# Performance work log

Hardware: AMD Instinct MI355X
Metric: run time of the kernel (lower is better)

## Reference

```python
import jax, jax.numpy as jnp
import numpy as np

N_NODES = 100000
D_IN, D_OUT = 1024, 512
B, K = 8192, 64


def setup_inputs() -> dict:
    key = jax.random.key(0)
    k1, k2, k3, k4, k5 = jax.random.split(key, 5)
    X = jax.random.normal(k1, (N_NODES, D_IN), dtype=jnp.float32)
    indices = jax.random.randint(k2, (B, K), 0, N_NODES)  # top-K PPR neighbor ids per batch node
    values = jax.random.uniform(k3, (B, K), dtype=jnp.float32)  # PPR weights
    W = jax.random.normal(k4, (D_IN, D_OUT), dtype=jnp.float32) / np.sqrt(D_IN)
    b = jax.random.normal(k5, (D_OUT,), dtype=jnp.float32)
    return {"X": X, "indices": indices, "values": values, "W": W, "b": b}


def reference(X, indices, values, W, b):
    # Sparse PPR branch. Original: encode only unique gathered rows, then
    # re-expand via inverse indices. Since the encoder is row-pointwise,
    # encoder(X[u_fwd])[u_bwd] == encoder(X)[indices]; we encode all nodes once
    # (n_nodes < B*K here) then gather -- identical math, jit-friendly.
    enc = X @ W + b                      # [N, d_out]
    gathered = enc[indices]              # [B, K, d_out]
    return jnp.einsum('bk,bkd->bd', values, gathered)  # weighted sum over K neighbors
```

## Files before the change

### kernel.cpp

```cpp
#include <hip/hip_runtime.h>

typedef unsigned short ushort_t;
typedef __bf16 bf16x8 __attribute__((ext_vector_type(8)));
typedef float f32x4 __attribute__((ext_vector_type(4)));

#define N_NODES 100000
#define D_IN    1024
#define D_OUT   512
#define B_SZ    8192
#define K_NB    64

__device__ __forceinline__ ushort_t f2bf(float f) {
    unsigned int u = __builtin_bit_cast(unsigned int, f);
    u += 0x7FFFu + ((u >> 16) & 1u);
    return (ushort_t)(u >> 16);
}

__global__ __launch_bounds__(256) void cast_w_kernel(
        const float* __restrict__ W, ushort_t* __restrict__ Wt) {
    int o = blockIdx.x * 256 + threadIdx.x;
    int n = o >> 10;
    int k = o & 1023;
    Wt[o] = f2bf(W[k * D_OUT + n]);
}

__global__ __launch_bounds__(256) void gather_kernel(
        const float* __restrict__ X, const int* __restrict__ idx,
        const float* __restrict__ val, ushort_t* __restrict__ Y,
        float* __restrict__ s) {
    int b = blockIdx.x;
    int t = threadIdx.x;

    __shared__ int   sidx[K_NB];
    __shared__ float sval[K_NB];
    if (t < K_NB) {
        sidx[t] = idx[b * K_NB + t];
        sval[t] = val[b * K_NB + t];
    }
    __syncthreads();

    float ax = 0.f, ay = 0.f, az = 0.f, aw = 0.f;
    #pragma unroll 8
    for (int k = 0; k < K_NB; k++) {
        const float4* row = (const float4*)(X + (size_t)sidx[k] * D_IN);
        float4 x = row[t];
        float  v = sval[k];
        ax = fmaf(v, x.x, ax);
        ay = fmaf(v, x.y, ay);
        az = fmaf(v, x.z, az);
        aw = fmaf(v, x.w, aw);
    }

    uint2 o;
    o.x = (unsigned)f2bf(ax) | ((unsigned)f2bf(ay) << 16);
    o.y = (unsigned)f2bf(az) | ((unsigned)f2bf(aw) << 16);
    *(uint2*)(Y + (size_t)b * D_IN + t * 4) = o;

    if (t == 0) {
        float sum = 0.f;
        #pragma unroll
        for (int k = 0; k < K_NB; k++) sum += sval[k];
        s[b] = sum;
    }
}

__global__ __launch_bounds__(256) void gemm_kernel(
        const ushort_t* __restrict__ Y, const ushort_t* __restrict__ Wt,
        const float* __restrict__ s, const float* __restrict__ bias,
        float* __restrict__ out) {
    const int Kdim = D_IN;
    int m0 = blockIdx.x * 128;
    int n0 = blockIdx.y * 128;
    int t = threadIdx.x;
    int lane = t & 63;
    int wave = t >> 6;
    int wm = (wave >> 1) * 64;
    int wn = (wave & 1) * 64;
    int quad = lane >> 4;
    int l16  = lane & 15;

    __shared__ __align__(16) ushort_t As[128 * 32];
    __shared__ __align__(16) ushort_t Bs[128 * 32];

    f32x4 acc[4][4];
    f32x4 zero = {0.f, 0.f, 0.f, 0.f};
    #pragma unroll
    for (int i = 0; i < 4; i++)
        #pragma unroll
        for (int j = 0; j < 4; j++)
            acc[i][j] = zero;

    for (int k0 = 0; k0 < Kdim; k0 += 32) {
        #pragma unroll
        for (int i = 0; i < 2; i++) {
            int c   = t + i * 256;
            int row = c >> 2;
            int chk = c & 3;
            *(int4*)(As + row * 32 + chk * 8) =
                *(const int4*)(Y + (size_t)(m0 + row) * Kdim + k0 + chk * 8);
            *(int4*)(Bs + row * 32 + chk * 8) =
                *(const int4*)(Wt + (size_t)(n0 + row) * Kdim + k0 + chk * 8);
        }
        __syncthreads();

        bf16x8 a[4], b[4];
        #pragma unroll
        for (int i = 0; i < 4; i++) {
            a[i] = *(const bf16x8*)(As + (wm + i * 16 + l16) * 32 + quad * 8);
            b[i] = *(const bf16x8*)(Bs + (wn + i * 16 + l16) * 32 + quad * 8);
        }
        #pragma unroll
        for (int i = 0; i < 4; i++)
            #pragma unroll
            for (int j = 0; j < 4; j++)
                acc[i][j] = __builtin_amdgcn_mfma_f32_16x16x32_bf16(
                                a[i], b[j], acc[i][j], 0, 0, 0);
        __syncthreads();
    }

    #pragma unroll
    for (int i = 0; i < 4; i++) {
        #pragma unroll
        for (int r = 0; r < 4; r++) {
            int grow = m0 + wm + i * 16 + quad * 4 + r;
            float sv = s[grow];
            #pragma unroll
            for (int j = 0; j < 4; j++) {
                int gcol = n0 + wn + j * 16 + l16;
                out[(size_t)grow * D_OUT + gcol] = acc[i][j][r] + sv * bias[gcol];
            }
        }
    }
}

extern "C" void kernel_launch(void* const* d_in, const int* in_sizes, int n_in,
                              void* d_out, int out_size, void* d_ws, size_t ws_size,
                              hipStream_t stream) {
    const float* X    = (const float*)d_in[0];
    const int*   idx  = (const int*)d_in[1];
    const float* val  = (const float*)d_in[2];
    const float* W    = (const float*)d_in[3];
    const float* bias = (const float*)d_in[4];
    float* out = (float*)d_out;

    char* ws = (char*)d_ws;
    ushort_t* Yb = (ushort_t*)ws;
    ushort_t* Wt = (ushort_t*)(ws + (size_t)B_SZ * D_IN * 2);
    float*    sb = (float*)(ws + (size_t)B_SZ * D_IN * 2
                               + (size_t)D_OUT * D_IN * 2);

    hipLaunchKernelGGL(cast_w_kernel, dim3((D_OUT * D_IN) / 256), dim3(256),
                       0, stream, W, Wt);
    hipLaunchKernelGGL(gather_kernel, dim3(B_SZ), dim3(256),
                       0, stream, X, idx, val, Yb, sb);
    hipLaunchKernelGGL(gemm_kernel, dim3(B_SZ / 128, D_OUT / 128), dim3(256),
                       0, stream, Yb, Wt, sb, bias, out);
}
```

Baseline: 777.8 us.

## Pre-cast X to bf16 before gathering and swizzle GEMM LDS layout

Adds a kernel that converts all of X to bf16 in workspace, then gathers bf16 rows with two half-blocks splitting the K neighbours and reducing through shared memory. Separately, the GEMM LDS tiles are XOR-swizzled to reduce bank conflicts. The cast reads all 400MB of X and writes 200MB, while the baseline gather only touches about 8192*64 rows (roughly 2GB of random reads, many of them repeats). The new path also rounds inputs to bf16 before accumulation and only runs when the workspace is large enough.

```diff
diff --git a/kernel.cpp b/kernel.cpp
--- a/kernel.cpp
+++ b/kernel.cpp
@@ -14,6 +14,12 @@
     unsigned int u = __builtin_bit_cast(unsigned int, f);
     u += 0x7FFFu + ((u >> 16) & 1u);
     return (ushort_t)(u >> 16);
+}
+__device__ __forceinline__ float bflo(unsigned d) {
+    return __builtin_bit_cast(float, d << 16);
+}
+__device__ __forceinline__ float bfhi(unsigned d) {
+    return __builtin_bit_cast(float, d & 0xFFFF0000u);
 }
 
 __global__ __launch_bounds__(256) void cast_w_kernel(
@@ -24,7 +30,79 @@
     Wt[o] = f2bf(W[k * D_OUT + n]);
 }
 
-__global__ __launch_bounds__(256) void gather_kernel(
+__global__ __launch_bounds__(256) void cast_x_kernel(
+        const float* __restrict__ X, ushort_t* __restrict__ Xb) {
+    size_t o = ((size_t)blockIdx.x * 256 + threadIdx.x) * 8;
+    float4 a = *(const float4*)(X + o);
+    float4 b = *(const float4*)(X + o + 4);
+    uint4 r;
+    r.x = (unsigned)f2bf(a.x) | ((unsigned)f2bf(a.y) << 16);
+    r.y = (unsigned)f2bf(a.z) | ((unsigned)f2bf(a.w) << 16);
+    r.z = (unsigned)f2bf(b.x) | ((unsigned)f2bf(b.y) << 16);
+    r.w = (unsigned)f2bf(b.z) | ((unsigned)f2bf(b.w) << 16);
+    *(uint4*)(Xb + o) = r;
+}
+
+__global__ __launch_bounds__(256) void gather_bf16_kernel(
+        const ushort_t* __restrict__ Xb, const int* __restrict__ idx,
+        const float* __restrict__ val, ushort_t* __restrict__ Y,
+        float* __restrict__ s) {
+    int b = blockIdx.x;
+    int t = threadIdx.x;
+
+    __shared__ int   sidx[K_NB];
+    __shared__ float sval[K_NB];
+    __shared__ float part[128 * 8];
+    if (t < K_NB) {
+        sidx[t] = idx[b * K_NB + t];
+        sval[t] = val[b * K_NB + t];
+    }
+    __syncthreads();
+
+    int h = t >> 7;
+    int c = t & 127;
+
+    float acc[8] = {0.f, 0.f, 0.f, 0.f, 0.f, 0.f, 0.f, 0.f};
+    #pragma unroll 4
+    for (int k = h; k < K_NB; k += 2) {
+        const uint4* row = (const uint4*)(Xb + (size_t)sidx[k] * D_IN);
+        uint4 x = row[c];
+        float v = sval[k];
+        acc[0] = fmaf(v, bflo(x.x), acc[0]);
+        acc[1] = fmaf(v, bfhi(x.x), acc[1]);
+        acc[2] = fmaf(v, bflo(x.y), acc[2]);
+        acc[3] = fmaf(v, bfhi(x.y), acc[3]);
+        acc[4] = fmaf(v, bflo(x.z), acc[4]);
+        acc[5] = fmaf(v, bfhi(x.z), acc[5]);
+        acc[6] = fmaf(v, bflo(x.w), acc[6]);
+        acc[7] = fmaf(v, bfhi(x.w), acc[7]);
+    }
+
+    if (h == 1) {
+        #pragma unroll
+        for (int e = 0; e < 8; e++) part[c * 8 + e] = acc[e];
+    }
+    __syncthreads();
+    if (h == 0) {
+        ushort_t r[8];
+        #pragma unroll
+        for (int e = 0; e < 8; e++) r[e] = f2bf(acc[e] + part[c * 8 + e]);
+        uint4 o;
+        o.x = (unsigned)r[0] | ((unsigned)r[1] << 16);
+        o.y = (unsigned)r[2] | ((unsigned)r[3] << 16);
+        o.z = (unsigned)r[4] | ((unsigned)r[5] << 16);
+        o.w = (unsigned)r[6] | ((unsigned)r[7] << 16);
+        *(uint4*)(Y + (size_t)b * D_IN + c * 8) = o;
+    }
+    if (t == 0) {
+        float sum = 0.f;
+        #pragma unroll
+        for (int k = 0; k < K_NB; k++) sum += sval[k];
+        s[b] = sum;
+    }
+}
+
+__global__ __launch_bounds__(256) void gather_f32_kernel(
         const float* __restrict__ X, const int* __restrict__ idx,
         const float* __restrict__ val, ushort_t* __restrict__ Y,
         float* __restrict__ s) {
@@ -50,7 +128,6 @@
         az = fmaf(v, x.z, az);
         aw = fmaf(v, x.w, aw);
     }
-
     uint2 o;
     o.x = (unsigned)f2bf(ax) | ((unsigned)f2bf(ay) << 16);
     o.y = (unsigned)f2bf(az) | ((unsigned)f2bf(aw) << 16);
@@ -90,24 +167,28 @@
         for (int j = 0; j < 4; j++)
             acc[i][j] = zero;
 
+    int rsw = (l16 >> 2) & 3;
+
     for (int k0 = 0; k0 < Kdim; k0 += 32) {
         #pragma unroll
         for (int i = 0; i < 2; i++) {
             int c   = t + i * 256;
             int row = c >> 2;
             int chk = c & 3;
-            *(int4*)(As + row * 32 + chk * 8) =
+            int pos = chk ^ ((row >> 2) & 3);
+            *(int4*)(As + row * 32 + pos * 8) =
                 *(const int4*)(Y + (size_t)(m0 + row) * Kdim + k0 + chk * 8);
-            *(int4*)(Bs + row * 32 + chk * 8) =
+            *(int4*)(Bs + row * 32 + pos * 8) =
                 *(const int4*)(Wt + (size_t)(n0 + row) * Kdim + k0 + chk * 8);
         }
         __syncthreads();
 
         bf16x8 a[4], b[4];
+        int rchk = quad ^ rsw;
         #pragma unroll
         for (int i = 0; i < 4; i++) {
-            a[i] = *(const bf16x8*)(As + (wm + i * 16 + l16) * 32 + quad * 8);
-            b[i] = *(const bf16x8*)(Bs + (wn + i * 16 + l16) * 32 + quad * 8);
+            a[i] = *(const bf16x8*)(As + (wm + i * 16 + l16) * 32 + rchk * 8);
+            b[i] = *(const bf16x8*)(Bs + (wn + i * 16 + l16) * 32 + rchk * 8);
         }
         #pragma unroll
         for (int i = 0; i < 4; i++)
@@ -143,16 +224,39 @@
     const float* bias = (const float*)d_in[4];
     float* out = (float*)d_out;
 
+    const size_t XB_BYTES = (size_t)N_NODES * D_IN * 2;
+    const size_t Y_BYTES  = (size_t)B_SZ * D_IN * 2;
+    const size_t WT_BYTES = (size_t)D_OUT * D_IN * 2;
+    const size_t S_BYTES  = (size_t)B_SZ * 4;
+
     char* ws = (char*)d_ws;
-    ushort_t* Yb = (ushort_t*)ws;
-    ushort_t* Wt = (ushort_t*)(ws + (size_t)B_SZ * D_IN * 2);
-    float*    sb = (float*)(ws + (size_t)B_SZ * D_IN * 2
-                               + (size_t)D_OUT * D_IN * 2);
+    bool fast = ws_size >= XB_BYTES + Y_BYTES + WT_BYTES + S_BYTES;
+
+    ushort_t *Xb, *Yb, *Wt;
+    float *sb;
+    if (fast) {
+        Xb = (ushort_t*)ws;
+        Yb = (ushort_t*)(ws + XB_BYTES);
+        Wt = (ushort_t*)(ws + XB_BYTES + Y_BYTES);
+        sb = (float*)(ws + XB_BYTES + Y_BYTES + WT_BYTES);
+    } else {
+        Xb = nullptr;
+        Yb = (ushort_t*)ws;
+        Wt = (ushort_t*)(ws + Y_BYTES);
+        sb = (float*)(ws + Y_BYTES + WT_BYTES);
+    }
 
     hipLaunchKernelGGL(cast_w_kernel, dim3((D_OUT * D_IN) / 256), dim3(256),
                        0, stream, W, Wt);
-    hipLaunchKernelGGL(gather_kernel, dim3(B_SZ), dim3(256),
-                       0, stream, X, idx, val, Yb, sb);
+    if (fast) {
+        hipLaunchKernelGGL(cast_x_kernel, dim3((N_NODES * D_IN) / (256 * 8)),
+                           dim3(256), 0, stream, X, Xb);
+        hipLaunchKernelGGL(gather_bf16_kernel, dim3(B_SZ), dim3(256),
+                           0, stream, Xb, idx, val, Yb, sb);
+    } else {
+        hipLaunchKernelGGL(gather_f32_kernel, dim3(B_SZ), dim3(256),
+                           0, stream, X, idx, val, Yb, sb);
+    }
     hipLaunchKernelGGL(gemm_kernel, dim3(B_SZ / 128, D_OUT / 128), dim3(256),
                        0, stream, Yb, Wt, sb, bias, out);
 }
```

Result: faster. 729.9 us (-6.2%).
